# Kernel tuning notes

Measured on AMD Instinct MI355X. Metric: run time of the kernel, lower is better.

## Reference

```python
import jax, jax.numpy as jnp
import numpy as np
from jax import lax

BN_EPS = 1e-3


def fps(xyz, npoint):
    """Farthest point sampling. xyz: (B,N,3) -> idx: (B, npoint) int32.
    Deterministic start at index 0 (torch version uses randint)."""
    B, N, _ = xyz.shape
    batch = jnp.arange(B)

    def step(carry, _):
        dist, farthest = carry                      # (B,N), (B,)
        centroid = xyz[batch, farthest]             # (B,3)
        d = jnp.sum((xyz - centroid[:, None, :]) ** 2, axis=-1)  # (B,N)
        dist = jnp.minimum(dist, d)
        nxt = jnp.argmax(dist, axis=-1)
        return (dist, nxt), farthest

    init = (jnp.full((B, N), 1e10, dtype=xyz.dtype), jnp.zeros((B,), dtype=jnp.int32))
    _, idx = lax.scan(step, init, None, length=npoint)  # (npoint, B)
    return idx.T                                        # (B, npoint)


def _bn(y, g, b, m, v):
    # eval-mode BatchNorm1d over channel axis (last)
    return (y - m) * (g * lax.rsqrt(v + BN_EPS)) + b


def setup_inputs() -> dict:
    key = jax.random.key(0)
    ks = jax.random.split(key, 16)
    B, N, C, S = 32, 8192, 64, 512
    cin, cout, hid = 3 + C, 2 * C, 8  # hidden = max(8, 128//16)
    xyz = jax.random.normal(ks[0], (B, N, 3), jnp.float32)
    feat = jax.random.normal(ks[1], (B, N, C), jnp.float32)
    sc = lambda fan: 1.0 / np.sqrt(fan)
    return {
        "xyz": xyz,
        "feat": feat,
        "W1": jax.random.normal(ks[2], (cout, cin), jnp.float32) * sc(cin),
        "g1": jnp.ones((cout,), jnp.float32),
        "b1": jnp.zeros((cout,), jnp.float32),
        "m1": jax.random.normal(ks[3], (cout,), jnp.float32) * 0.1,
        "v1": jax.random.uniform(ks[4], (cout,), jnp.float32) + 0.5,
        "W2": jax.random.normal(ks[5], (cout, cout), jnp.float32) * sc(cout),
        "g2": jnp.ones((cout,), jnp.float32),
        "b2": jnp.zeros((cout,), jnp.float32),
        "m2": jax.random.normal(ks[6], (cout,), jnp.float32) * 0.1,
        "v2": jax.random.uniform(ks[7], (cout,), jnp.float32) + 0.5,
        "Wproj": jax.random.normal(ks[8], (cout, cin), jnp.float32) * sc(cin),
        "Wse1": jax.random.normal(ks[9], (hid, cout), jnp.float32) * sc(cout),
        "bse1": jnp.zeros((hid,), jnp.float32),
        "Wse2": jax.random.normal(ks[10], (cout, hid), jnp.float32) * sc(hid),
        "bse2": jnp.zeros((cout,), jnp.float32),
        "npoint": S,
    }


def reference(xyz, feat, W1, g1, b1, m1, v1, W2, g2, b2, m2, v2,
              Wproj, Wse1, bse1, Wse2, bse2, npoint):
    # FPS + gather (the irregular-access part)
    idx = fps(xyz, npoint)                                     # (B,S)
    xyz_s = jnp.take_along_axis(xyz, idx[..., None], axis=1)   # (B,S,3)
    feat_s = jnp.take_along_axis(feat, idx[..., None], axis=1) # (B,S,C)
    x = jnp.concatenate([xyz_s, feat_s], axis=-1)              # (B,S,cin)

    # ResMLP1D: conv1x1 -> BN -> ReLU -> conv1x1 -> BN, then SE, residual, ReLU
    h = jax.nn.relu(_bn(jnp.einsum('bsc,oc->bso', x, W1), g1, b1, m1, v1))
    h = _bn(jnp.einsum('bsc,oc->bso', h, W2), g2, b2, m2, v2)  # (B,S,cout)

    # SE1D: global average pool over points, 2-layer bottleneck, sigmoid gate
    s = h.mean(axis=1)                                         # (B,cout)
    s = jax.nn.relu(s @ Wse1.T + bse1)
    s = jax.nn.sigmoid(s @ Wse2.T + bse2)
    h = h * s[:, None, :]

    out = jax.nn.relu(h + jnp.einsum('bsc,oc->bso', x, Wproj))
    return out
```

## Files before the change

kernel.cpp:

```cpp
#include <hip/hip_runtime.h>
#include <math.h>

#define B_ 32
#define N_ 8192
#define C_ 64
#define S_ 512
#define CIN 67
#define COUT 128

template <int CTRL>
__device__ __forceinline__ unsigned dppmov(unsigned v) {
  return (unsigned)__builtin_amdgcn_update_dpp(0, (int)v, CTRL, 0xF, 0xF, true);
}
template <int CTRL>
__device__ __forceinline__ float dppmaxf(float v) {
  return fmaxf(v, __uint_as_float(dppmov<CTRL>(__float_as_uint(v))));
}

__global__ __launch_bounds__(512)
void fps_kernel(const float* __restrict__ xyz, int* __restrict__ idx_out) {
  __shared__ float lx[N_], ly[N_], lz[N_];
  __shared__ __align__(16) float sM[2][8];
  __shared__ __align__(16) int sI[2][8];
  __shared__ int idxl[S_];
  const int b = blockIdx.x;
  const int t = threadIdx.x;
  const float* base = xyz + (size_t)b * N_ * 3;
  #pragma unroll
  for (int k = 0; k < 12; ++k) {
    int j = k * 512 + t;
    float4 v = ((const float4*)base)[j];
    int f = j * 4;
    float vals[4] = {v.x, v.y, v.z, v.w};
    #pragma unroll
    for (int e = 0; e < 4; ++e) {
      int ff = f + e;
      int p = ff / 3;
      int c = ff - p * 3;
      if (c == 0) lx[p] = vals[e];
      else if (c == 1) ly[p] = vals[e];
      else lz[p] = vals[e];
    }
  }
  __syncthreads();
  const int p0 = t * 16;
  float px[16], py[16], pz[16], dist[16];
  #pragma unroll
  for (int j = 0; j < 16; ++j) {
    px[j] = lx[p0 + j];
    py[j] = ly[p0 + j];
    pz[j] = lz[p0 + j];
    dist[j] = 1e10f;
  }
  int bidx = 0;
  float cx = lx[0], cy = ly[0], cz = lz[0];
  const int w = t >> 6;
  const int lane = t & 63;

  for (int s = 0; s < S_; ++s) {
    const int par = s & 1;
    if (t == 0) idxl[s] = bidx;
    float gv[2];
    int gi[2];
    #pragma unroll
    for (int g = 0; g < 2; ++g) {
      gv[g] = -1.0f;
      gi[g] = 0;
      #pragma unroll
      for (int u = 0; u < 8; ++u) {
        const int j = g * 8 + u;
        float dx = __fsub_rn(px[j], cx);
        float dy = __fsub_rn(py[j], cy);
        float dz = __fsub_rn(pz[j], cz);
        float d = __fadd_rn(__fadd_rn(__fmul_rn(dx, dx), __fmul_rn(dy, dy)),
                            __fmul_rn(dz, dz));
        d = fminf(dist[j], d);
        dist[j] = d;
        if (d > gv[g]) { gv[g] = d; gi[g] = j; }
      }
    }
    float bestv = gv[0];
    int bj = gi[0];
    if (gv[1] > bestv) { bestv = gv[1]; bj = gi[1]; }
    float m = bestv;
    m = dppmaxf<0x111>(m);
    m = dppmaxf<0x112>(m);
    m = dppmaxf<0x114>(m);
    m = dppmaxf<0x118>(m);
    m = dppmaxf<0x142>(m);
    m = dppmaxf<0x143>(m);
    const float M = __uint_as_float(
        (unsigned)__builtin_amdgcn_readlane((int)__float_as_uint(m), 63));
    const unsigned long long ball = __ballot(bestv == M);
    const int l0 = __ffsll(ball) - 1;
    const int bj0 = __builtin_amdgcn_readlane(bj, l0);
    const int widx = ((w << 6) | l0) * 16 + bj0;
    if (lane == 0) { sM[par][w] = M; sI[par][w] = widx; }
    __syncthreads();
    const float4 ma = *(const float4*)&sM[par][0];
    const float4 mb = *(const float4*)&sM[par][4];
    const int4 ia = *(const int4*)&sI[par][0];
    const int4 ib = *(const int4*)&sI[par][4];
    const float mm = fmaxf(fmaxf(fmaxf(ma.x, ma.y), fmaxf(ma.z, ma.w)),
                           fmaxf(fmaxf(mb.x, mb.y), fmaxf(mb.z, mb.w)));
    int nb = ib.w;
    nb = (mb.z == mm) ? ib.z : nb;
    nb = (mb.y == mm) ? ib.y : nb;
    nb = (mb.x == mm) ? ib.x : nb;
    nb = (ma.w == mm) ? ia.w : nb;
    nb = (ma.z == mm) ? ia.z : nb;
    nb = (ma.y == mm) ? ia.y : nb;
    nb = (ma.x == mm) ? ia.x : nb;
    bidx = nb;
    cx = lx[bidx]; cy = ly[bidx]; cz = lz[bidx];
  }
  if (t < S_) idx_out[b * S_ + t] = idxl[t];
}

__global__ __launch_bounds__(256) void mlp_kernel(
    const float* __restrict__ xyz, const float* __restrict__ feat,
    const float* __restrict__ W1, const float* __restrict__ g1,
    const float* __restrict__ b1, const float* __restrict__ m1,
    const float* __restrict__ v1, const float* __restrict__ W2,
    const float* __restrict__ g2, const float* __restrict__ b2,
    const float* __restrict__ m2, const float* __restrict__ v2,
    const float* __restrict__ Wproj, const int* __restrict__ idx,
    float* __restrict__ h2buf, float* __restrict__ partials,
    float* __restrict__ projbuf) {
  __shared__ float xs[CIN][64];
  __shared__ float hs[COUT][64];
  __shared__ float wlds[COUT][COUT];
  __shared__ float psums[8][COUT];
  const int blk = blockIdx.x;
  const int b = blk >> 3, tile = blk & 7;
  const int t = threadIdx.x;

  {
    const int p = t >> 2, q = t & 3;
    const int pid = idx[b * S_ + tile * 64 + p];
    const float* frow = feat + ((size_t)(b * N_ + pid)) * C_ + q * 16;
    #pragma unroll
    for (int i = 0; i < 4; ++i) {
      float4 v = ((const float4*)frow)[i];
      xs[3 + q * 16 + i * 4 + 0][p] = v.x;
      xs[3 + q * 16 + i * 4 + 1][p] = v.y;
      xs[3 + q * 16 + i * 4 + 2][p] = v.z;
      xs[3 + q * 16 + i * 4 + 3][p] = v.w;
    }
    if (q == 0) {
      const float* xr = xyz + ((size_t)(b * N_ + pid)) * 3;
      xs[0][p] = xr[0]; xs[1][p] = xr[1]; xs[2][p] = xr[2];
    }
  }
  for (int f = t; f < COUT * CIN; f += 256) {
    int o = f / CIN, k = f - o * CIN;
    wlds[k][o] = W1[f];
  }
  __syncthreads();

  const int py = t >> 5, ox = t & 31;
  const int py8 = py * 8, ox4 = ox * 4;
  float acc[8][4];

  #pragma unroll
  for (int i = 0; i < 8; ++i)
    #pragma unroll
    for (int j = 0; j < 4; ++j) acc[i][j] = 0.0f;
  for (int k = 0; k < CIN; ++k) {
    float4 xa = *(const float4*)&xs[k][py8];
    float4 xb = *(const float4*)&xs[k][py8 + 4];
    float4 wv = *(const float4*)&wlds[k][ox4];
    float xv[8] = {xa.x, xa.y, xa.z, xa.w, xb.x, xb.y, xb.z, xb.w};
    float wr[4] = {wv.x, wv.y, wv.z, wv.w};
    #pragma unroll
    for (int i = 0; i < 8; ++i)
      #pragma unroll
      for (int j = 0; j < 4; ++j) acc[i][j] = fmaf(xv[i], wr[j], acc[i][j]);
  }
  #pragma unroll
  for (int j = 0; j < 4; ++j) {
    const int o = ox4 + j;
    const float sc = g1[o] * (1.0f / sqrtf(v1[o] + 1e-3f));
    const float sh = b1[o] - m1[o] * sc;
    #pragma unroll
    for (int i = 0; i < 8; ++i)
      hs[o][py8 + i] = fmaxf(fmaf(acc[i][j], sc, sh), 0.0f);
  }
  __syncthreads();
  for (int f = t; f < COUT * COUT; f += 256) {
    int o = f >> 7, k = f & 127;
    wlds[k][o] = W2[f];
  }
  __syncthreads();

  #pragma unroll
  for (int i = 0; i < 8; ++i)
    #pragma unroll
    for (int j = 0; j < 4; ++j) acc[i][j] = 0.0f;
  for (int k = 0; k < COUT; ++k) {
    float4 xa = *(const float4*)&hs[k][py8];
    float4 xb = *(const float4*)&hs[k][py8 + 4];
    float4 wv = *(const float4*)&wlds[k][ox4];
    float xv[8] = {xa.x, xa.y, xa.z, xa.w, xb.x, xb.y, xb.z, xb.w};
    float wr[4] = {wv.x, wv.y, wv.z, wv.w};
    #pragma unroll
    for (int i = 0; i < 8; ++i)
      #pragma unroll
      for (int j = 0; j < 4; ++j) acc[i][j] = fmaf(xv[i], wr[j], acc[i][j]);
  }
  {
    float sc[4], sh[4], sume[4];
    #pragma unroll
    for (int j = 0; j < 4; ++j) {
      const int o = ox4 + j;
      sc[j] = g2[o] * (1.0f / sqrtf(v2[o] + 1e-3f));
      sh[j] = b2[o] - m2[o] * sc[j];
      sume[j] = 0.0f;
    }
    const int basept = b * S_ + tile * 64 + py8;
    #pragma unroll
    for (int i = 0; i < 8; ++i) {
      float4 hv;
      hv.x = fmaf(acc[i][0], sc[0], sh[0]);
      hv.y = fmaf(acc[i][1], sc[1], sh[1]);
      hv.z = fmaf(acc[i][2], sc[2], sh[2]);
      hv.w = fmaf(acc[i][3], sc[3], sh[3]);
      sume[0] += hv.x; sume[1] += hv.y; sume[2] += hv.z; sume[3] += hv.w;
      *(float4*)&h2buf[((size_t)(basept + i)) * COUT + ox4] = hv;
    }
    *(float4*)&psums[py][ox4] = make_float4(sume[0], sume[1], sume[2], sume[3]);
  }
  __syncthreads();
  if (t < COUT) {
    float sacc = 0.0f;
    #pragma unroll
    for (int r = 0; r < 8; ++r) sacc += psums[r][t];
    partials[(b * 8 + tile) * COUT + t] = sacc;
  }
  for (int f = t; f < COUT * CIN; f += 256) {
    int o = f / CIN, k = f - o * CIN;
    wlds[k][o] = Wproj[f];
  }
  __syncthreads();

  #pragma unroll
  for (int i = 0; i < 8; ++i)
    #pragma unroll
    for (int j = 0; j < 4; ++j) acc[i][j] = 0.0f;
  for (int k = 0; k < CIN; ++k) {
    float4 xa = *(const float4*)&xs[k][py8];
    float4 xb = *(const float4*)&xs[k][py8 + 4];
    float4 wv = *(const float4*)&wlds[k][ox4];
    float xv[8] = {xa.x, xa.y, xa.z, xa.w, xb.x, xb.y, xb.z, xb.w};
    float wr[4] = {wv.x, wv.y, wv.z, wv.w};
    #pragma unroll
    for (int i = 0; i < 8; ++i)
      #pragma unroll
      for (int j = 0; j < 4; ++j) acc[i][j] = fmaf(xv[i], wr[j], acc[i][j]);
  }
  {
    const int basept = b * S_ + tile * 64 + py8;
    #pragma unroll
    for (int i = 0; i < 8; ++i) {
      float4 pv = make_float4(acc[i][0], acc[i][1], acc[i][2], acc[i][3]);
      *(float4*)&projbuf[((size_t)(basept + i)) * COUT + ox4] = pv;
    }
  }
}

__global__ __launch_bounds__(128) void se_kernel(
    const float* __restrict__ partials, const float* __restrict__ Wse1,
    const float* __restrict__ bse1, const float* __restrict__ Wse2,
    const float* __restrict__ bse2, float* __restrict__ sgate) {
  __shared__ float mv[COUT];
  __shared__ float rv[8];
  const int b = blockIdx.x;
  const int t = threadIdx.x;
  float s = 0.0f;
  #pragma unroll
  for (int r = 0; r < 8; ++r) s += partials[(b * 8 + r) * COUT + t];
  mv[t] = s * (1.0f / (float)S_);
  __syncthreads();
  if (t < 8) {
    float a = bse1[t];
    for (int o = 0; o < COUT; ++o) a = fmaf(mv[o], Wse1[t * COUT + o], a);
    rv[t] = fmaxf(a, 0.0f);
  }
  __syncthreads();
  float a = bse2[t];
  #pragma unroll
  for (int h = 0; h < 8; ++h) a = fmaf(rv[h], Wse2[t * 8 + h], a);
  sgate[b * COUT + t] = 1.0f / (1.0f + expf(-a));
}

__global__ __launch_bounds__(256) void finish_kernel(
    const float* __restrict__ h2buf, const float* __restrict__ sgate,
    float* __restrict__ out) {
  const int i = blockIdx.x * 256 + threadIdx.x;
  const int total = B_ * S_ * COUT / 4;
  if (i >= total) return;
  const int fo = i & 31;
  const int row = i >> 5;
  const int b = row >> 9;
  float4 h = ((const float4*)h2buf)[i];
  float4 g = ((const float4*)sgate)[b * 32 + fo];
  float4 p = ((float4*)out)[i];
  float4 r;
  r.x = fmaxf(fmaf(h.x, g.x, p.x), 0.0f);
  r.y = fmaxf(fmaf(h.y, g.y, p.y), 0.0f);
  r.z = fmaxf(fmaf(h.z, g.z, p.z), 0.0f);
  r.w = fmaxf(fmaf(h.w, g.w, p.w), 0.0f);
  ((float4*)out)[i] = r;
}

extern "C" void kernel_launch(void* const* d_in, const int* in_sizes, int n_in,
                              void* d_out, int out_size, void* d_ws, size_t ws_size,
                              hipStream_t stream) {
  const float* xyz   = (const float*)d_in[0];
  const float* feat  = (const float*)d_in[1];
  const float* W1    = (const float*)d_in[2];
  const float* g1    = (const float*)d_in[3];
  const float* b1    = (const float*)d_in[4];
  const float* m1    = (const float*)d_in[5];
  const float* v1    = (const float*)d_in[6];
  const float* W2    = (const float*)d_in[7];
  const float* g2    = (const float*)d_in[8];
  const float* b2    = (const float*)d_in[9];
  const float* m2    = (const float*)d_in[10];
  const float* v2    = (const float*)d_in[11];
  const float* Wproj = (const float*)d_in[12];
  const float* Wse1  = (const float*)d_in[13];
  const float* bse1  = (const float*)d_in[14];
  const float* Wse2  = (const float*)d_in[15];
  const float* bse2  = (const float*)d_in[16];
  float* out = (float*)d_out;

  char* ws = (char*)d_ws;
  int*   idx      = (int*)ws;
  float* h2buf    = (float*)(ws + (64 << 10));
  float* partials = (float*)(ws + (64 << 10) + B_ * S_ * COUT * 4);
  float* sgate    = (float*)(ws + (64 << 10) + B_ * S_ * COUT * 4 +
                             B_ * 8 * COUT * 4);

  fps_kernel<<<B_, 512, 0, stream>>>(xyz, idx);
  mlp_kernel<<<B_ * 8, 256, 0, stream>>>(xyz, feat, W1, g1, b1, m1, v1,
                                         W2, g2, b2, m2, v2, Wproj, idx,
                                         h2buf, partials, out);
  se_kernel<<<B_, 128, 0, stream>>>(partials, Wse1, bse1, Wse2, bse2, sgate);
  finish_kernel<<<(B_ * S_ * COUT / 4 + 255) / 256, 256, 0, stream>>>(h2buf, sgate, out);
}
```

Measured before the change: 532.4 us.

## Replace per-iteration block barrier in FPS with epoch-tagged packed atomic slots

Each wave writes a 64-bit key packing the iteration number, the non-negative max distance bits and the inverted point index into an LDS slot. All threads then spin on relaxed loads until all eight slots carry the current epoch, and take the max key as the argmax. This removes the __syncthreads per FPS step and merges the value and index into one comparison. The risk is spin-wait cost and correctness that depends on relaxed LDS ordering and the double-buffered slots not being overwritten early.

After: 623.2 us. 17.1% more time.

```diff
diff --git a/kernel.cpp b/kernel.cpp
--- a/kernel.cpp
+++ b/kernel.cpp
@@ -20,8 +20,7 @@
 __global__ __launch_bounds__(512)
 void fps_kernel(const float* __restrict__ xyz, int* __restrict__ idx_out) {
   __shared__ float lx[N_], ly[N_], lz[N_];
-  __shared__ __align__(16) float sM[2][8];
-  __shared__ __align__(16) int sI[2][8];
+  __shared__ __align__(16) unsigned long long slots[2][8];
   __shared__ int idxl[S_];
   const int b = blockIdx.x;
   const int t = threadIdx.x;
@@ -42,6 +41,7 @@
       else lz[p] = vals[e];
     }
   }
+  if (t < 16) ((unsigned long long*)slots)[t] = 0ull;
   __syncthreads();
   const int p0 = t * 16;
   float px[16], py[16], pz[16], dist[16];
@@ -82,38 +82,46 @@
     float bestv = gv[0];
     int bj = gi[0];
     if (gv[1] > bestv) { bestv = gv[1]; bj = gi[1]; }
-    float m = bestv;
-    m = dppmaxf<0x111>(m);
-    m = dppmaxf<0x112>(m);
-    m = dppmaxf<0x114>(m);
-    m = dppmaxf<0x118>(m);
-    m = dppmaxf<0x142>(m);
-    m = dppmaxf<0x143>(m);
+    float mx = bestv;
+    mx = dppmaxf<0x111>(mx);
+    mx = dppmaxf<0x112>(mx);
+    mx = dppmaxf<0x114>(mx);
+    mx = dppmaxf<0x118>(mx);
+    mx = dppmaxf<0x142>(mx);
+    mx = dppmaxf<0x143>(mx);
     const float M = __uint_as_float(
-        (unsigned)__builtin_amdgcn_readlane((int)__float_as_uint(m), 63));
+        (unsigned)__builtin_amdgcn_readlane((int)__float_as_uint(mx), 63));
     const unsigned long long ball = __ballot(bestv == M);
     const int l0 = __ffsll(ball) - 1;
     const int bj0 = __builtin_amdgcn_readlane(bj, l0);
     const int widx = ((w << 6) | l0) * 16 + bj0;
-    if (lane == 0) { sM[par][w] = M; sI[par][w] = widx; }
-    __syncthreads();
-    const float4 ma = *(const float4*)&sM[par][0];
-    const float4 mb = *(const float4*)&sM[par][4];
-    const int4 ia = *(const int4*)&sI[par][0];
-    const int4 ib = *(const int4*)&sI[par][4];
-    const float mm = fmaxf(fmaxf(fmaxf(ma.x, ma.y), fmaxf(ma.z, ma.w)),
-                           fmaxf(fmaxf(mb.x, mb.y), fmaxf(mb.z, mb.w)));
-    int nb = ib.w;
-    nb = (mb.z == mm) ? ib.z : nb;
-    nb = (mb.y == mm) ? ib.y : nb;
-    nb = (mb.x == mm) ? ib.x : nb;
-    nb = (ma.w == mm) ? ia.w : nb;
-    nb = (ma.z == mm) ? ia.z : nb;
-    nb = (ma.y == mm) ? ia.y : nb;
-    nb = (ma.x == mm) ? ia.x : nb;
-    bidx = nb;
+    const unsigned long long key =
+        ((unsigned long long)(s + 1) << 46) |
+        ((unsigned long long)__float_as_uint(M < 0.0f ? 0.0f : M) << 14) |
+        (unsigned long long)(16383 - widx);
+    if (lane == 0)
+      __hip_atomic_store(&slots[par][w], key, __ATOMIC_RELAXED,
+                         __HIP_MEMORY_SCOPE_WORKGROUP);
+    const unsigned long long want = (unsigned long long)(s + 1) << 46;
+    unsigned long long kk[8];
+    unsigned long long mis;
+    do {
+      mis = 0;
+      #pragma unroll
+      for (int q = 0; q < 8; ++q) {
+        kk[q] = __hip_atomic_load(&slots[par][q], __ATOMIC_RELAXED,
+                                  __HIP_MEMORY_SCOPE_WORKGROUP);
+        mis |= (kk[q] ^ want) >> 46;
+      }
+    } while (mis != 0);
+    unsigned long long best = kk[0];
+    #pragma unroll
+    for (int q = 1; q < 8; ++q)
+      if (kk[q] > best) best = kk[q];
+    bidx = 16383 - (int)(unsigned)(best & 0x3FFFull);
     cx = lx[bidx]; cy = ly[bidx]; cz = lz[bidx];
   }
+  __syncthreads();
   if (t < S_) idx_out[b * S_ + t] = idxl[t];
 }
 
```
